# Kernel optimization log

Measured on AMD Instinct MI355X. Metric: run time of the kernel, lower is better.

Reference implementation:

```python
import jax, jax.numpy as jnp
import numpy as np

N_NODES = 100000
N_EDGES = 2000000
N_GRAPHS = 2000
IN_DIM = 7
EDGE_DIM = 4
HID = 32
N_CLASSES = 2
NEG_SLOPE = 0.2
BN_EPS = 1e-5


def setup_inputs() -> dict:
    key = jax.random.key(0)
    ks = jax.random.split(key, 16)
    x = jax.random.normal(ks[0], (N_NODES, IN_DIM), dtype=jnp.float32)
    edge_index = jax.random.randint(ks[1], (2, N_EDGES), 0, N_NODES, dtype=jnp.int64)
    batch = jnp.sort(jax.random.randint(ks[2], (N_NODES,), 0, N_GRAPHS, dtype=jnp.int64))
    edge_attr = jax.random.normal(ks[3], (N_EDGES, EDGE_DIM), dtype=jnp.float32)
    s = 0.1
    W0 = jax.random.normal(ks[4], (IN_DIM, HID), dtype=jnp.float32) * s
    W12 = jax.random.normal(ks[5], (2, HID, HID), dtype=jnp.float32) * s
    att_src = jax.random.normal(ks[6], (3, HID), dtype=jnp.float32) * s
    att_dst = jax.random.normal(ks[7], (3, HID), dtype=jnp.float32) * s
    lin_edge = jax.random.normal(ks[8], (3, EDGE_DIM, HID), dtype=jnp.float32) * s
    att_edge = jax.random.normal(ks[9], (3, HID), dtype=jnp.float32) * s
    bias = jnp.zeros((3, HID), dtype=jnp.float32)
    bn_gamma = jnp.ones((3, HID), dtype=jnp.float32)
    bn_beta = jnp.zeros((3, HID), dtype=jnp.float32)
    fc_W = jax.random.normal(ks[10], (HID, N_CLASSES), dtype=jnp.float32) * s
    fc_b = jnp.zeros((N_CLASSES,), dtype=jnp.float32)
    return dict(x=x, edge_index=edge_index, batch=batch, edge_attr=edge_attr,
                W0=W0, W12=W12, att_src=att_src, att_dst=att_dst,
                lin_edge=lin_edge, att_edge=att_edge, bias=bias,
                bn_gamma=bn_gamma, bn_beta=bn_beta, fc_W=fc_W, fc_b=fc_b)


def gat_layer(x, src, dst, edge_attr, W, a_src, a_dst, We, a_edge, b):
    # PyG GATConv, heads=1, add_self_loops=False: edge_attr conditions attention only.
    N = x.shape[0]
    h = x @ W                                   # [N, H]
    e = edge_attr @ We                          # [E, H]
    score = ((h * a_src).sum(-1)[src]
             + (h * a_dst).sum(-1)[dst]
             + (e * a_edge).sum(-1))            # [E]
    score = jax.nn.leaky_relu(score, NEG_SLOPE)
    m = jax.ops.segment_max(score, dst, num_segments=N)
    w = jnp.exp(score - m[dst])
    denom = jax.ops.segment_sum(w, dst, num_segments=N)
    alpha = w / (denom[dst] + 1e-16)            # segment softmax over incoming edges
    out = jax.ops.segment_sum(h[src] * alpha[:, None], dst, num_segments=N)
    return out + b


def batchnorm(x, gamma, beta):
    mu = x.mean(axis=0)
    var = ((x - mu) ** 2).mean(axis=0)          # biased var, as torch BN normalization
    return (x - mu) * jax.lax.rsqrt(var + BN_EPS) * gamma + beta


def reference(x, edge_index, batch, edge_attr, W0, W12, att_src, att_dst,
              lin_edge, att_edge, bias, bn_gamma, bn_beta, fc_W, fc_b):
    src, dst = edge_index[0], edge_index[1]
    Ws = [W0, W12[0], W12[1]]
    h = x
    for l in range(3):
        h = gat_layer(h, src, dst, edge_attr, Ws[l], att_src[l], att_dst[l],
                      lin_edge[l], att_edge[l], bias[l])
        h = batchnorm(h, bn_gamma[l], bn_beta[l])
        h = jax.nn.relu(h)
    node_embs = h
    graph_emb = jax.ops.segment_sum(node_embs, batch, num_segments=N_GRAPHS)
    out = graph_emb @ fc_W + fc_b
    return (out, node_embs, graph_emb)
```

## Files before the change

### kernel.cpp

```cpp
#include <hip/hip_runtime.h>
#include <math.h>

#define N_NODES   100000
#define N_EDGES   2000000
#define N_GRAPHS  2000
#define IN_DIM    7
#define EDGE_DIM  4
#define HID       32
#define N_CLASSES 2
#define NEG_SLOPE 0.2f
#define BN_EPS    1e-5f

__global__ void k_ce_all(const float* __restrict__ lin_edge, const float* __restrict__ att_edge,
                         float* __restrict__ ce3, float* __restrict__ gsum3,
                         float* __restrict__ gsq3) {
    int t = threadIdx.x;
    if (t < 12) {
        int l = t >> 2, d = t & 3;
        float s = 0.f;
        for (int k = 0; k < HID; ++k)
            s += lin_edge[(size_t)l * EDGE_DIM * HID + d * HID + k] * att_edge[l * HID + k];
        ce3[t] = s;
    }
    if (t < 3 * HID) { gsum3[t] = 0.f; gsq3[t] = 0.f; }
}

__global__ void k_hist(const int* __restrict__ dst, int* __restrict__ deg) {
    int e = blockIdx.x * blockDim.x + threadIdx.x;
    if (e < N_EDGES) atomicAdd(deg + dst[e], 1);
}

__global__ void k_scan(const int* __restrict__ deg, int* __restrict__ offs,
                       int* __restrict__ cursor) {
    __shared__ int wsum[16];
    __shared__ int carry;
    int t = threadIdx.x, lane = t & 63, w = t >> 6;
    if (t == 0) carry = 0;
    __syncthreads();
    for (int base = 0; base < N_NODES; base += 1024) {
        int i = base + t;
        int v = (i < N_NODES) ? deg[i] : 0;
        int x = v;
#pragma unroll
        for (int o = 1; o < 64; o <<= 1) {
            int y = __shfl_up(x, o, 64);
            if (lane >= o) x += y;
        }
        if (lane == 63) wsum[w] = x;
        __syncthreads();
        if (t < 16) {
            int s = wsum[t];
#pragma unroll
            for (int o = 1; o < 16; o <<= 1) {
                int y = __shfl_up(s, o, 16);
                if (t >= o) s += y;
            }
            wsum[t] = s;
        }
        __syncthreads();
        int wpref = (w == 0) ? 0 : wsum[w - 1];
        int excl = carry + wpref + x - v;
        if (i < N_NODES) { offs[i] = excl; cursor[i] = excl; }
        __syncthreads();
        if (t == 0) carry += wsum[15];
        __syncthreads();
    }
}

__global__ void k_scatter(const int* __restrict__ src, const int* __restrict__ dst,
                          const float4* __restrict__ eattr, const float* __restrict__ ce3,
                          int* __restrict__ cursor, int4* __restrict__ pack) {
    int e = blockIdx.x * blockDim.x + threadIdx.x;
    if (e >= N_EDGES) return;
    float4 ea = eattr[e];
    float e0 = ea.x * ce3[0] + ea.y * ce3[1] + ea.z * ce3[2] + ea.w * ce3[3];
    float e1 = ea.x * ce3[4] + ea.y * ce3[5] + ea.z * ce3[6] + ea.w * ce3[7];
    float e2 = ea.x * ce3[8] + ea.y * ce3[9] + ea.z * ce3[10] + ea.w * ce3[11];
    int d = dst[e];
    int pos = atomicAdd(cursor + d, 1);
    pack[pos] = make_int4(src[e], __float_as_int(e0), __float_as_int(e1), __float_as_int(e2));
}

template <int INDIM, bool BN>
__global__ void k_linear(const float* __restrict__ in, const float* __restrict__ W,
                         const float* __restrict__ a_src, const float* __restrict__ a_dst,
                         const float* __restrict__ gsum, const float* __restrict__ gsq,
                         const float* __restrict__ gamma, const float* __restrict__ beta,
                         float* __restrict__ h, float* __restrict__ asrc,
                         float* __restrict__ adst) {
    __shared__ float Ws[INDIM * HID];
    for (int i = threadIdx.x; i < INDIM * HID; i += blockDim.x) Ws[i] = W[i];
    __syncthreads();
    int g = threadIdx.x >> 5, k = threadIdx.x & 31;
    int n = blockIdx.x * 8 + g;
    if (n >= N_NODES) return;
    float xv;
    if (BN) {
        const float invN = 1.f / (float)N_NODES;
        float mu = gsum[k] * invN;
        float var = gsq[k] * invN - mu * mu;
        var = fmaxf(var, 0.f);
        float scl = rsqrtf(var + BN_EPS) * gamma[k];
        float v = (in[(size_t)n * INDIM + k] - mu) * scl + beta[k];
        xv = fmaxf(v, 0.f);
    } else {
        xv = (k < INDIM) ? in[(size_t)n * INDIM + k] : 0.f;
    }
    float acc = 0.f;
#pragma unroll
    for (int d = 0; d < INDIM; ++d) acc += __shfl(xv, d, 32) * Ws[d * HID + k];
    h[(size_t)n * HID + k] = acc;
    float vs = acc * a_src[k];
    float vd = acc * a_dst[k];
#pragma unroll
    for (int m = 16; m > 0; m >>= 1) {
        vs += __shfl_xor(vs, m, 32);
        vd += __shfl_xor(vd, m, 32);
    }
    if (k == 0) { asrc[n] = vs; adst[n] = vd; }
}

template <int L>
__global__ void k_aggr(const int4* __restrict__ pack, const int* __restrict__ offs,
                       const int* __restrict__ endp, const float* __restrict__ h,
                       const float* __restrict__ asrc, const float* __restrict__ adst,
                       const float* __restrict__ bias, float* __restrict__ out,
                       float* __restrict__ gsum, float* __restrict__ gsq) {
    __shared__ float ssum[HID], ssq[HID];
    if (threadIdx.x < HID) { ssum[threadIdx.x] = 0.f; ssq[threadIdx.x] = 0.f; }
    __syncthreads();
    int g = threadIdx.x >> 5, k = threadIdx.x & 31;
    int n = blockIdx.x * 8 + g;
    if (n < N_NODES) {
        int pbeg = offs[n], en = endp[n];
        float ad = adst[n];
        float den = 0.f, a = 0.f;
        for (int p = pbeg; p < en; p += 8) {
            int4 pk[8];
            float as[8], hh[8], w[8];
#pragma unroll
            for (int j = 0; j < 8; ++j) {
                int q = p + j;
                q = q < en ? q : en - 1;
                pk[j] = pack[q];
            }
#pragma unroll
            for (int j = 0; j < 8; ++j) as[j] = asrc[pk[j].x];
#pragma unroll
            for (int j = 0; j < 8; ++j) hh[j] = h[(size_t)pk[j].x * HID + k];
#pragma unroll
            for (int j = 0; j < 8; ++j) {
                float edot = __int_as_float(L == 0 ? pk[j].y : (L == 1 ? pk[j].z : pk[j].w));
                float sc = as[j] + ad + edot;
                sc = sc > 0.f ? sc : NEG_SLOPE * sc;
                w[j] = (p + j < en) ? __expf(sc) : 0.f;
            }
#pragma unroll
            for (int j = 0; j < 8; ++j) {
                den += w[j];
                a = fmaf(w[j], hh[j], a);
            }
        }
        float v = a / (den + 1e-16f) + bias[k];
        out[(size_t)n * HID + k] = v;
        atomicAdd(&ssum[k], v);
        atomicAdd(&ssq[k], v * v);
    }
    __syncthreads();
    if (threadIdx.x < HID) {
        atomicAdd(gsum + threadIdx.x, ssum[threadIdx.x]);
        atomicAdd(gsq + threadIdx.x, ssq[threadIdx.x]);
    }
}

__global__ void k_bn_relu_pool(const float* __restrict__ acc, const float* __restrict__ gsum,
                               const float* __restrict__ gsq, const float* __restrict__ gamma,
                               const float* __restrict__ beta, const int* __restrict__ batch,
                               float* __restrict__ nemb, float* __restrict__ gemb) {
    int g = threadIdx.x >> 5, k = threadIdx.x & 31;
    int n = blockIdx.x * 8 + g;
    if (n >= N_NODES) return;
    const float invN = 1.f / (float)N_NODES;
    float mu = gsum[k] * invN;
    float var = gsq[k] * invN - mu * mu;
    var = fmaxf(var, 0.f);
    float scl = rsqrtf(var + BN_EPS) * gamma[k];
    float v = (acc[(size_t)n * HID + k] - mu) * scl + beta[k];
    v = fmaxf(v, 0.f);
    nemb[(size_t)n * HID + k] = v;
    atomicAdd(gemb + (size_t)batch[n] * HID + k, v);
}

__global__ void k_fc(const float* __restrict__ gemb, const float* __restrict__ W,
                     const float* __restrict__ b, float* __restrict__ out) {
    int g = blockIdx.x * blockDim.x + threadIdx.x;
    if (g >= N_GRAPHS) return;
    float a0 = b[0], a1 = b[1];
    for (int k = 0; k < HID; ++k) {
        float v = gemb[(size_t)g * HID + k];
        a0 += v * W[k * 2 + 0];
        a1 += v * W[k * 2 + 1];
    }
    out[g * 2 + 0] = a0;
    out[g * 2 + 1] = a1;
}

extern "C" void kernel_launch(void* const* d_in, const int* in_sizes, int n_in,
                              void* d_out, int out_size, void* d_ws, size_t ws_size,
                              hipStream_t stream) {
    const float* x        = (const float*)d_in[0];
    const int*   ei       = (const int*)d_in[1];
    const int*   batch    = (const int*)d_in[2];
    const float* eattr    = (const float*)d_in[3];
    const float* W0       = (const float*)d_in[4];
    const float* W12      = (const float*)d_in[5];
    const float* att_src  = (const float*)d_in[6];
    const float* att_dst  = (const float*)d_in[7];
    const float* lin_edge = (const float*)d_in[8];
    const float* att_edge = (const float*)d_in[9];
    const float* bias     = (const float*)d_in[10];
    const float* bn_gamma = (const float*)d_in[11];
    const float* bn_beta  = (const float*)d_in[12];
    const float* fc_W     = (const float*)d_in[13];
    const float* fc_b     = (const float*)d_in[14];

    const int* srcA = ei;
    const int* dstA = ei + N_EDGES;

    float* out       = (float*)d_out;
    float* node_embs = out + N_GRAPHS * N_CLASSES;
    float* graph_emb = node_embs + (size_t)N_NODES * HID;

    char* ws = (char*)d_ws;
    size_t off = 0;
    auto alloc = [&](size_t bytes) { char* p = ws + off; off += (bytes + 255) & ~(size_t)255; return p; };
    float* hT    = (float*)alloc((size_t)N_NODES * HID * 4);
    float* A0    = (float*)alloc((size_t)N_NODES * HID * 4);
    float* A1    = (float*)alloc((size_t)N_NODES * HID * 4);
    int4*  pack  = (int4*)alloc((size_t)N_EDGES * 16);
    int*   deg   = (int*)alloc((size_t)N_NODES * 4);
    int*   offs  = (int*)alloc((size_t)N_NODES * 4);
    int*   cursor= (int*)alloc((size_t)N_NODES * 4);
    float* asrc  = (float*)alloc((size_t)N_NODES * 4);
    float* adst  = (float*)alloc((size_t)N_NODES * 4);
    float* ce3   = (float*)alloc(12 * 4);
    float* gsum3 = (float*)alloc(3 * HID * 4);
    float* gsq3  = (float*)alloc(3 * HID * 4);
    (void)ws_size;

    const int nodeBlocks = (N_NODES + 7) / 8;
    const int edgeBlocks = (N_EDGES + 255) / 256;

    hipMemsetAsync(deg, 0, (size_t)N_NODES * 4, stream);
    k_ce_all<<<1, 128, 0, stream>>>(lin_edge, att_edge, ce3, gsum3, gsq3);
    k_hist<<<edgeBlocks, 256, 0, stream>>>(dstA, deg);
    k_scan<<<1, 1024, 0, stream>>>(deg, offs, cursor);
    k_scatter<<<edgeBlocks, 256, 0, stream>>>(srcA, dstA, (const float4*)eattr, ce3, cursor, pack);

    k_linear<IN_DIM, false><<<nodeBlocks, 256, 0, stream>>>(
        x, W0, att_src, att_dst, nullptr, nullptr, nullptr, nullptr, hT, asrc, adst);
    k_aggr<0><<<nodeBlocks, 256, 0, stream>>>(pack, offs, cursor, hT, asrc, adst,
                                              bias, A0, gsum3, gsq3);
    k_linear<HID, true><<<nodeBlocks, 256, 0, stream>>>(
        A0, W12, att_src + HID, att_dst + HID, gsum3, gsq3, bn_gamma, bn_beta, hT, asrc, adst);
    k_aggr<1><<<nodeBlocks, 256, 0, stream>>>(pack, offs, cursor, hT, asrc, adst,
                                              bias + HID, A1, gsum3 + HID, gsq3 + HID);
    k_linear<HID, true><<<nodeBlocks, 256, 0, stream>>>(
        A1, W12 + HID * HID, att_src + 2 * HID, att_dst + 2 * HID,
        gsum3 + HID, gsq3 + HID, bn_gamma + HID, bn_beta + HID, hT, asrc, adst);
    k_aggr<2><<<nodeBlocks, 256, 0, stream>>>(pack, offs, cursor, hT, asrc, adst,
                                              bias + 2 * HID, A0, gsum3 + 2 * HID, gsq3 + 2 * HID);

    hipMemsetAsync(graph_emb, 0, (size_t)N_GRAPHS * HID * 4, stream);
    k_bn_relu_pool<<<nodeBlocks, 256, 0, stream>>>(A0, gsum3 + 2 * HID, gsq3 + 2 * HID,
                                                   bn_gamma + 2 * HID, bn_beta + 2 * HID,
                                                   batch, node_embs, graph_emb);
    k_fc<<<(N_GRAPHS + 255) / 256, 256, 0, stream>>>(graph_emb, fc_W, fc_b, out);
}
```

Baseline: 1.020 ms.

## Parallelize CSR scan, store features in bf16, split edges across wave halves with prefetch

Replaces the single-block serial prefix scan with a three-kernel multi-block scan. Node features h are stored as bf16 to halve gather traffic in the aggregation kernels. Each aggregation now assigns a full 64-lane wave per node, with the two 32-lane halves taking alternating edges, and prefetches the next packed-edge batch in software. The aim is to cut the serial scan latency and the memory-bound gather cost, at the price of bf16 rounding in the aggregated features and extra launches.

New measurement: 1.400 ms. 37.3% more time.

```diff
diff --git a/kernel.cpp b/kernel.cpp
--- a/kernel.cpp
+++ b/kernel.cpp
@@ -1,4 +1,5 @@
 #include <hip/hip_runtime.h>
+#include <hip/hip_bf16.h>
 #include <math.h>
 
 #define N_NODES   100000
@@ -10,6 +11,7 @@
 #define N_CLASSES 2
 #define NEG_SLOPE 0.2f
 #define BN_EPS    1e-5f
+#define SCAN_B    1024
 
 __global__ void k_ce_all(const float* __restrict__ lin_edge, const float* __restrict__ att_edge,
                          float* __restrict__ ce3, float* __restrict__ gsum3,
@@ -30,40 +32,49 @@
     if (e < N_EDGES) atomicAdd(deg + dst[e], 1);
 }
 
-__global__ void k_scan(const int* __restrict__ deg, int* __restrict__ offs,
-                       int* __restrict__ cursor) {
+__global__ void k_scan1(const int* __restrict__ deg, int* __restrict__ offs,
+                        int* __restrict__ bsum) {
     __shared__ int wsum[16];
-    __shared__ int carry;
     int t = threadIdx.x, lane = t & 63, w = t >> 6;
-    if (t == 0) carry = 0;
-    __syncthreads();
-    for (int base = 0; base < N_NODES; base += 1024) {
-        int i = base + t;
-        int v = (i < N_NODES) ? deg[i] : 0;
-        int x = v;
-#pragma unroll
-        for (int o = 1; o < 64; o <<= 1) {
-            int y = __shfl_up(x, o, 64);
-            if (lane >= o) x += y;
-        }
-        if (lane == 63) wsum[w] = x;
-        __syncthreads();
-        if (t < 16) {
-            int s = wsum[t];
-#pragma unroll
-            for (int o = 1; o < 16; o <<= 1) {
-                int y = __shfl_up(s, o, 16);
-                if (t >= o) s += y;
-            }
-            wsum[t] = s;
-        }
-        __syncthreads();
-        int wpref = (w == 0) ? 0 : wsum[w - 1];
-        int excl = carry + wpref + x - v;
-        if (i < N_NODES) { offs[i] = excl; cursor[i] = excl; }
-        __syncthreads();
-        if (t == 0) carry += wsum[15];
-        __syncthreads();
+    int i = blockIdx.x * SCAN_B + t;
+    int v = (i < N_NODES) ? deg[i] : 0;
+    int x = v;
+#pragma unroll
+    for (int o = 1; o < 64; o <<= 1) { int y = __shfl_up(x, o, 64); if (lane >= o) x += y; }
+    if (lane == 63) wsum[w] = x;
+    __syncthreads();
+    if (t < 16) {
+        int s = wsum[t];
+#pragma unroll
+        for (int o = 1; o < 16; o <<= 1) { int y = __shfl_up(s, o, 16); if (t >= o) s += y; }
+        wsum[t] = s;
+    }
+    __syncthreads();
+    int excl = (w ? wsum[w - 1] : 0) + x - v;
+    if (i < N_NODES) offs[i] = excl;
+    if (t == 0) bsum[blockIdx.x] = wsum[15];
+}
+
+__global__ void k_scan2(int* __restrict__ bsum, int nb) {
+    __shared__ int w0;
+    int t = threadIdx.x, lane = t & 63, w = t >> 6;
+    int v = (t < nb) ? bsum[t] : 0;
+    int x = v;
+#pragma unroll
+    for (int o = 1; o < 64; o <<= 1) { int y = __shfl_up(x, o, 64); if (lane >= o) x += y; }
+    if (w == 0 && lane == 63) w0 = x;
+    __syncthreads();
+    int excl = x - v + (w ? w0 : 0);
+    if (t < nb) bsum[t] = excl;
+}
+
+__global__ void k_scan3(int* __restrict__ offs, const int* __restrict__ bsum,
+                        int* __restrict__ cursor) {
+    int i = blockIdx.x * SCAN_B + threadIdx.x;
+    if (i < N_NODES) {
+        int o = offs[i] + bsum[blockIdx.x];
+        offs[i] = o;
+        cursor[i] = o;
     }
 }
 
@@ -86,7 +97,7 @@
                          const float* __restrict__ a_src, const float* __restrict__ a_dst,
                          const float* __restrict__ gsum, const float* __restrict__ gsq,
                          const float* __restrict__ gamma, const float* __restrict__ beta,
-                         float* __restrict__ h, float* __restrict__ asrc,
+                         __hip_bfloat16* __restrict__ h, float* __restrict__ asrc,
                          float* __restrict__ adst) {
     __shared__ float Ws[INDIM * HID];
     for (int i = threadIdx.x; i < INDIM * HID; i += blockDim.x) Ws[i] = W[i];
@@ -109,7 +120,7 @@
     float acc = 0.f;
 #pragma unroll
     for (int d = 0; d < INDIM; ++d) acc += __shfl(xv, d, 32) * Ws[d * HID + k];
-    h[(size_t)n * HID + k] = acc;
+    h[(size_t)n * HID + k] = __float2bfloat16(acc);
     float vs = acc * a_src[k];
     float vd = acc * a_dst[k];
 #pragma unroll
@@ -122,49 +133,70 @@
 
 template <int L>
 __global__ void k_aggr(const int4* __restrict__ pack, const int* __restrict__ offs,
-                       const int* __restrict__ endp, const float* __restrict__ h,
+                       const int* __restrict__ endp, const __hip_bfloat16* __restrict__ hb,
                        const float* __restrict__ asrc, const float* __restrict__ adst,
                        const float* __restrict__ bias, float* __restrict__ out,
                        float* __restrict__ gsum, float* __restrict__ gsq) {
     __shared__ float ssum[HID], ssq[HID];
     if (threadIdx.x < HID) { ssum[threadIdx.x] = 0.f; ssq[threadIdx.x] = 0.f; }
     __syncthreads();
-    int g = threadIdx.x >> 5, k = threadIdx.x & 31;
-    int n = blockIdx.x * 8 + g;
+    int lane = threadIdx.x & 63;
+    int half = lane >> 5;
+    int k = lane & 31;
+    int wv = threadIdx.x >> 6;
+    int n = blockIdx.x * 4 + wv;
     if (n < N_NODES) {
         int pbeg = offs[n], en = endp[n];
         float ad = adst[n];
         float den = 0.f, a = 0.f;
-        for (int p = pbeg; p < en; p += 8) {
-            int4 pk[8];
-            float as[8], hh[8], w[8];
+        if (pbeg < en) {
+            int4 pkn[8];
+            int p = pbeg;
 #pragma unroll
             for (int j = 0; j < 8; ++j) {
-                int q = p + j;
+                int q = p + 2 * j + half;
                 q = q < en ? q : en - 1;
-                pk[j] = pack[q];
+                pkn[j] = pack[q];
             }
-#pragma unroll
-            for (int j = 0; j < 8; ++j) as[j] = asrc[pk[j].x];
-#pragma unroll
-            for (int j = 0; j < 8; ++j) hh[j] = h[(size_t)pk[j].x * HID + k];
-#pragma unroll
-            for (int j = 0; j < 8; ++j) {
-                float edot = __int_as_float(L == 0 ? pk[j].y : (L == 1 ? pk[j].z : pk[j].w));
-                float sc = as[j] + ad + edot;
-                sc = sc > 0.f ? sc : NEG_SLOPE * sc;
-                w[j] = (p + j < en) ? __expf(sc) : 0.f;
-            }
-#pragma unroll
-            for (int j = 0; j < 8; ++j) {
-                den += w[j];
-                a = fmaf(w[j], hh[j], a);
+            while (p < en) {
+                int4 pk[8];
+#pragma unroll
+                for (int j = 0; j < 8; ++j) pk[j] = pkn[j];
+                int pn = p + 16;
+                if (pn < en) {
+#pragma unroll
+                    for (int j = 0; j < 8; ++j) {
+                        int q = pn + 2 * j + half;
+                        q = q < en ? q : en - 1;
+                        pkn[j] = pack[q];
+                    }
+                }
+                float as[8], hh[8];
+#pragma unroll
+                for (int j = 0; j < 8; ++j) as[j] = asrc[pk[j].x];
+#pragma unroll
+                for (int j = 0; j < 8; ++j)
+                    hh[j] = __bfloat162float(hb[(size_t)pk[j].x * HID + k]);
+#pragma unroll
+                for (int j = 0; j < 8; ++j) {
+                    float edot = __int_as_float(L == 0 ? pk[j].y : (L == 1 ? pk[j].z : pk[j].w));
+                    float sc = as[j] + ad + edot;
+                    sc = sc > 0.f ? sc : NEG_SLOPE * sc;
+                    float w = (p + 2 * j + half < en) ? __expf(sc) : 0.f;
+                    den += w;
+                    a = fmaf(w, hh[j], a);
+                }
+                p = pn;
             }
         }
-        float v = a / (den + 1e-16f) + bias[k];
-        out[(size_t)n * HID + k] = v;
-        atomicAdd(&ssum[k], v);
-        atomicAdd(&ssq[k], v * v);
+        den += __shfl_xor(den, 32, 64);
+        a   += __shfl_xor(a, 32, 64);
+        if (half == 0) {
+            float v = a / (den + 1e-16f) + bias[k];
+            out[(size_t)n * HID + k] = v;
+            atomicAdd(&ssum[k], v);
+            atomicAdd(&ssq[k], v * v);
+        }
     }
     __syncthreads();
     if (threadIdx.x < HID) {
@@ -234,13 +266,14 @@
     char* ws = (char*)d_ws;
     size_t off = 0;
     auto alloc = [&](size_t bytes) { char* p = ws + off; off += (bytes + 255) & ~(size_t)255; return p; };
-    float* hT    = (float*)alloc((size_t)N_NODES * HID * 4);
+    __hip_bfloat16* hT = (__hip_bfloat16*)alloc((size_t)N_NODES * HID * 2);
     float* A0    = (float*)alloc((size_t)N_NODES * HID * 4);
     float* A1    = (float*)alloc((size_t)N_NODES * HID * 4);
     int4*  pack  = (int4*)alloc((size_t)N_EDGES * 16);
     int*   deg   = (int*)alloc((size_t)N_NODES * 4);
     int*   offs  = (int*)alloc((size_t)N_NODES * 4);
     int*   cursor= (int*)alloc((size_t)N_NODES * 4);
+    int*   bsum  = (int*)alloc(128 * 4);
     float* asrc  = (float*)alloc((size_t)N_NODES * 4);
     float* adst  = (float*)alloc((size_t)N_NODES * 4);
     float* ce3   = (float*)alloc(12 * 4);
@@ -248,32 +281,36 @@
     float* gsq3  = (float*)alloc(3 * HID * 4);
     (void)ws_size;
 
-    const int nodeBlocks = (N_NODES + 7) / 8;
-    const int edgeBlocks = (N_EDGES + 255) / 256;
+    const int nodeBlocks8 = (N_NODES + 7) / 8;
+    const int nodeBlocks4 = (N_NODES + 3) / 4;
+    const int edgeBlocks  = (N_EDGES + 255) / 256;
+    const int scanBlocks  = (N_NODES + SCAN_B - 1) / SCAN_B;
 
     hipMemsetAsync(deg, 0, (size_t)N_NODES * 4, stream);
     k_ce_all<<<1, 128, 0, stream>>>(lin_edge, att_edge, ce3, gsum3, gsq3);
     k_hist<<<edgeBlocks, 256, 0, stream>>>(dstA, deg);
-    k_scan<<<1, 1024, 0, stream>>>(deg, offs, cursor);
+    k_scan1<<<scanBlocks, SCAN_B, 0, stream>>>(deg, offs, bsum);
+    k_scan2<<<1, 128, 0, stream>>>(bsum, scanBlocks);
+    k_scan3<<<scanBlocks, SCAN_B, 0, stream>>>(offs, bsum, cursor);
     k_scatter<<<edgeBlocks, 256, 0, stream>>>(srcA, dstA, (const float4*)eattr, ce3, cursor, pack);
 
-    k_linear<IN_DIM, false><<<nodeBlocks, 256, 0, stream>>>(
+    k_linear<IN_DIM, false><<<nodeBlocks8, 256, 0, stream>>>(
         x, W0, att_src, att_dst, nullptr, nullptr, nullptr, nullptr, hT, asrc, adst);
-    k_aggr<0><<<nodeBlocks, 256, 0, stream>>>(pack, offs, cursor, hT, asrc, adst,
-                                              bias, A0, gsum3, gsq3);
-    k_linear<HID, true><<<nodeBlocks, 256, 0, stream>>>(
+    k_aggr<0><<<nodeBlocks4, 256, 0, stream>>>(pack, offs, cursor, hT, asrc, adst,
+                                               bias, A0, gsum3, gsq3);
+    k_linear<HID, true><<<nodeBlocks8, 256, 0, stream>>>(
         A0, W12, att_src + HID, att_dst + HID, gsum3, gsq3, bn_gamma, bn_beta, hT, asrc, adst);
-    k_aggr<1><<<nodeBlocks, 256, 0, stream>>>(pack, offs, cursor, hT, asrc, adst,
-                                              bias + HID, A1, gsum3 + HID, gsq3 + HID);
-    k_linear<HID, true><<<nodeBlocks, 256, 0, stream>>>(
+    k_aggr<1><<<nodeBlocks4, 256, 0, stream>>>(pack, offs, cursor, hT, asrc, adst,
+                                               bias + HID, A1, gsum3 + HID, gsq3 + HID);
+    k_linear<HID, true><<<nodeBlocks8, 256, 0, stream>>>(
         A1, W12 + HID * HID, att_src + 2 * HID, att_dst + 2 * HID,
         gsum3 + HID, gsq3 + HID, bn_gamma + HID, bn_beta + HID, hT, asrc, adst);
-    k_aggr<2><<<nodeBlocks, 256, 0, stream>>>(pack, offs, cursor, hT, asrc, adst,
-                                              bias + 2 * HID, A0, gsum3 + 2 * HID, gsq3 + 2 * HID);
+    k_aggr<2><<<nodeBlocks4, 256, 0, stream>>>(pack, offs, cursor, hT, asrc, adst,
+                                               bias + 2 * HID, A0, gsum3 + 2 * HID, gsq3 + 2 * HID);
 
     hipMemsetAsync(graph_emb, 0, (size_t)N_GRAPHS * HID * 4, stream);
-    k_bn_relu_pool<<<nodeBlocks, 256, 0, stream>>>(A0, gsum3 + 2 * HID, gsq3 + 2 * HID,
-                                                   bn_gamma + 2 * HID, bn_beta + 2 * HID,
-                                                   batch, node_embs, graph_emb);
+    k_bn_relu_pool<<<nodeBlocks8, 256, 0, stream>>>(A0, gsum3 + 2 * HID, gsq3 + 2 * HID,
+                                                    bn_gamma + 2 * HID, bn_beta + 2 * HID,
+                                                    batch, node_embs, graph_emb);
     k_fc<<<(N_GRAPHS + 255) / 256, 256, 0, stream>>>(graph_emb, fc_W, fc_b, out);
 }
```
